# Kernel tuning notes

Hardware: AMD Instinct MI355X
Metric: run time of the kernel (lower is better)

Reference implementation:

```python
import jax, jax.numpy as jnp
import numpy as np

B, H, W, C = 2, 128, 128, 256
WS = 8            # current_window (query window)
KW = 16           # halo_window = 2*current_window
HEADS = 8
HD = C // HEADS
PRETRAIN = 8
CPB_HIDDEN = 512


def _rel_bias_consts():
    halo = (KW - WS) // 2
    coords = np.arange(1 - WS - halo, WS + halo, dtype=np.float32)  # length WS+KW-1 = 23
    tab = np.stack(np.meshgrid(coords, coords, indexing='ij'), axis=-1)  # [23,23,2]
    tab = tab * (8.0 / (PRETRAIN - 1.0))
    tab = np.sign(tab) * np.log1p(np.abs(tab)) / np.log(8.0)
    tab = tab.reshape(-1, 2).astype(np.float32)                      # [529,2]
    qi = np.arange(WS)
    qg = np.stack(np.meshgrid(qi, qi, indexing='ij')).reshape(2, -1)  # [2,64]
    ki = np.arange(KW)
    kg = np.stack(np.meshgrid(ki, ki, indexing='ij')).reshape(2, -1)  # [2,256]
    rel = qg[:, :, None] - kg[:, None] + (KW - 1)
    idx = (rel[0] * (WS + KW - 1) + rel[1]).reshape(-1).astype(np.int32)  # [64*256]
    return tab, idx

_REL_TAB, _REL_IDX = _rel_bias_consts()


def setup_inputs() -> dict:
    key = jax.random.key(0)
    ks = jax.random.split(key, 12)
    s = 0.02
    return {
        'x': jax.random.normal(ks[0], (B, H, W, C), jnp.float32),
        'w_qkv': jax.random.normal(ks[1], (C, 3 * C), jnp.float32) * s,
        'w_dw': jax.random.normal(ks[2], (3, 3, 1, 3 * C), jnp.float32) * s,  # depthwise HWIO
        'ln_g': jnp.ones((3 * C,), jnp.float32),
        'ln_b': jnp.zeros((3 * C,), jnp.float32),
        'q_bias': jnp.zeros((C,), jnp.float32),
        'v_bias': jnp.zeros((C,), jnp.float32),
        'logit_scale': jnp.full((HEADS, 1, 1), np.log(10.0), jnp.float32),
        'cpb_w1': jax.random.normal(ks[3], (2, CPB_HIDDEN), jnp.float32) * s,
        'cpb_b1': jnp.zeros((CPB_HIDDEN,), jnp.float32),
        'cpb_w2': jax.random.normal(ks[4], (CPB_HIDDEN, HEADS), jnp.float32) * s,
        'w_proj': jax.random.normal(ks[5], (C, C), jnp.float32) * s,
    }


def _l2n(t):
    # tf.math.l2_normalize with epsilon=1.55e-5
    return t * jax.lax.rsqrt(jnp.maximum(jnp.sum(t * t, -1, keepdims=True), 1.55e-5))


def reference(x, w_qkv, w_dw, ln_g, ln_b, q_bias, v_bias, logit_scale,
              cpb_w1, cpb_b1, cpb_w2, w_proj):
    nWh, nWw = H // WS, W // WS
    nW = nWh * nWw
    # qkv 1x1 conv + depthwise 3x3 + layernorm + (q,0,v) bias
    qkv = jnp.einsum('bhwc,cd->bhwd', x, w_qkv)
    qkv = jax.lax.conv_general_dilated(
        qkv, w_dw, (1, 1), 'SAME',
        dimension_numbers=('NHWC', 'HWIO', 'NHWC'), feature_group_count=3 * C)
    mu = jnp.mean(qkv, -1, keepdims=True)
    var = jnp.var(qkv, -1, keepdims=True)
    qkv = (qkv - mu) * jax.lax.rsqrt(var + 1e-5) * ln_g + ln_b
    qkv = qkv + jnp.concatenate([q_bias, jnp.zeros_like(q_bias), v_bias])
    q, kv = qkv[..., :C], qkv[..., C:]
    # window partition of q: [B*nW, heads, WS*WS, HD]
    qp = q.reshape(B, nWh, WS, nWw, WS, HEADS, HD)
    qp = qp.transpose(0, 1, 3, 5, 2, 4, 6).reshape(B * nW, HEADS, WS * WS, HD)
    # halo partition of kv: overlapping KWxKW patches, stride WS
    halo = (KW - WS) // 2
    kvp = jnp.pad(kv, ((0, 0), (halo, halo), (halo, halo), (0, 0)))
    ridx = (np.arange(nWh) * WS)[:, None] + np.arange(KW)[None]  # [nWh,KW]
    cidx = (np.arange(nWw) * WS)[:, None] + np.arange(KW)[None]  # [nWw,KW]
    kvp = kvp[:, ridx][:, :, :, cidx]               # [B,nWh,KW,nWw,KW,2C]
    kvp = kvp.transpose(0, 1, 3, 2, 4, 5).reshape(B * nW, KW * KW, 2, HEADS, HD)
    k = kvp[:, :, 0].transpose(0, 2, 1, 3)          # [B*nW, heads, KW*KW, HD]
    v = kvp[:, :, 1].transpose(0, 2, 1, 3)
    # cosine attention with clamped learned log-scale
    scale = jnp.exp(jnp.minimum(logit_scale, np.float32(np.log(100.0))))
    attn = jnp.einsum('whqd,whkd->whqk', _l2n(qp) * scale, _l2n(k))
    # continuous relative position bias (CPB MLP + gather)
    hidden = jax.nn.relu(jnp.asarray(_REL_TAB) @ cpb_w1 + cpb_b1)
    bias_tab = jax.nn.sigmoid(hidden @ cpb_w2) * 16.0        # [529, heads]
    rb = bias_tab[_REL_IDX].reshape(WS * WS, KW * KW, HEADS).transpose(2, 0, 1)
    attn = jax.nn.softmax(attn + rb[None], axis=-1)
    out = jnp.einsum('whqk,whkd->whqd', attn, v)             # [B*nW, heads, 64, HD]
    # reverse window partition
    out = out.reshape(B, nWh, nWw, HEADS, WS, WS, HD)
    out = out.transpose(0, 1, 4, 2, 5, 3, 6).reshape(B, H, W, C)
    return jnp.einsum('bhwc,cd->bhwd', out, w_proj)
```

## Files before the change

kernel.cpp:

```cpp
#include <hip/hip_runtime.h>
#include <hip/hip_bf16.h>
#include <hip/hip_fp16.h>
#include <cstddef>
#include <cstdint>

#define BB 2
#define HH 128
#define WW 128
#define CC 256
#define WSZ 8
#define KWIN 16
#define NHEADS 8
#define HD 32
#define C3 768
#define NPIX 32768
#define NWIN 512

typedef short    bf16x8 __attribute__((ext_vector_type(8)));
typedef _Float16 half8  __attribute__((ext_vector_type(8)));
typedef float    f32x4  __attribute__((ext_vector_type(4)));

#define LOG2E 1.4426950408889634f

#if __has_builtin(__builtin_amdgcn_exp2f)
#define EXP2(x) __builtin_amdgcn_exp2f(x)
#else
#define EXP2(x) __expf((x) * 0.6931471805599453f)
#endif

__device__ inline void gload_lds16(const _Float16* g, _Float16* l) {
    __builtin_amdgcn_global_load_lds(
        (const __attribute__((address_space(1))) unsigned int*)g,
        (__attribute__((address_space(3))) unsigned int*)l, 16, 0, 0);
}

__global__ __launch_bounds__(64) void cpb_kernel(const float* __restrict__ w1,
                                                 const float* __restrict__ b1,
                                                 const float* __restrict__ w2,
                                                 float* __restrict__ btab) {
    const int e = blockIdx.x;
    const int i = e / 23, j = e % 23;
    const float inv_log8 = 1.0f / logf(8.0f);
    float c0 = (float)(i - 11) * (8.0f / 7.0f);
    float c1 = (float)(j - 11) * (8.0f / 7.0f);
    float f0 = copysignf(log1pf(fabsf(c0)) * inv_log8, c0);
    float f1 = copysignf(log1pf(fabsf(c1)) * inv_log8, c1);

    const int t = threadIdx.x;
    float acc[8] = {0.f,0.f,0.f,0.f,0.f,0.f,0.f,0.f};
    for (int kk = 0; kk < 8; kk++) {
        int k = kk * 64 + t;
        float hid = f0 * w1[k] + f1 * w1[512 + k] + b1[k];
        hid = fmaxf(hid, 0.f);
        #pragma unroll
        for (int h = 0; h < 8; h++) acc[h] += hid * w2[k * 8 + h];
    }
    #pragma unroll
    for (int h = 0; h < 8; h++) {
        #pragma unroll
        for (int off = 32; off >= 1; off >>= 1) acc[h] += __shfl_xor(acc[h], off);
    }
    if (t < 8) {
        float v = acc[t];
        btab[e * 8 + t] = 16.0f / (1.0f + expf(-v));
    }
}

__global__ __launch_bounds__(256) void cvt_wdw(const float* __restrict__ src,
                                               _Float16* __restrict__ dst) {
    int i = blockIdx.x * 256 + threadIdx.x;
    if (i < 9 * C3) dst[i] = (_Float16)src[i];
}

__global__ __launch_bounds__(256) void transpose_cvt(const float* __restrict__ src,
                                                     _Float16* __restrict__ dst,
                                                     int R, int Cn) {
    __shared__ float t[32][33];
    const int bx = blockIdx.x, by = blockIdx.y;
    const int tx = threadIdx.x & 31, ty = threadIdx.x >> 5;
    #pragma unroll
    for (int i = 0; i < 4; i++) {
        int r = by * 32 + ty + i * 8;
        t[ty + i * 8][tx] = src[(size_t)r * Cn + bx * 32 + tx];
    }
    __syncthreads();
    #pragma unroll
    for (int i = 0; i < 4; i++) {
        int dr = bx * 32 + ty + i * 8;
        dst[(size_t)dr * R + by * 32 + tx] = (_Float16)t[tx][ty + i * 8];
    }
}

template <typename OT>
__global__ __launch_bounds__(256) void gemm_f16(const _Float16* __restrict__ A,
                                                const _Float16* __restrict__ Bt,
                                                OT* __restrict__ C,
                                                int M, int N, int K) {
    __shared__ _Float16 Ash[128][64];
    __shared__ _Float16 Bsh[128][64];
    const int tid = threadIdx.x;
    const int wv = tid >> 6, ln = tid & 63;
    const int quad = ln >> 4, l15 = ln & 15;
    const int rowb = blockIdx.y * 128;
    const int colb = blockIdx.x * 128;
    const int wm = (wv >> 1) * 64, wn = (wv & 1) * 64;

    const int r8 = ln >> 3, g = ln & 7;
    const int kg = g ^ r8;

    f32x4 acc[4][4] = {};
    for (int k0 = 0; k0 < K; k0 += 64) {
        #pragma unroll
        for (int i = 0; i < 4; i++) {
            const int m = wv * 32 + i * 8 + r8;
            gload_lds16(A + (size_t)(rowb + m) * K + k0 + kg * 8,
                        &Ash[wv * 32 + i * 8][0]);
            gload_lds16(Bt + (size_t)(colb + m) * K + k0 + kg * 8,
                        &Bsh[wv * 32 + i * 8][0]);
        }
        __syncthreads();
        #pragma unroll
        for (int kk = 0; kk < 2; kk++) {
            const int phys = ((kk * 4 + quad) ^ (l15 & 7)) * 8;
            half8 a[4], b[4];
            #pragma unroll
            for (int i = 0; i < 4; i++)
                a[i] = *(const half8*)&Ash[wm + i * 16 + l15][phys];
            #pragma unroll
            for (int j = 0; j < 4; j++)
                b[j] = *(const half8*)&Bsh[wn + j * 16 + l15][phys];
            #pragma unroll
            for (int i = 0; i < 4; i++)
                #pragma unroll
                for (int j = 0; j < 4; j++)
                    acc[i][j] = __builtin_amdgcn_mfma_f32_16x16x32_f16(
                        a[i], b[j], acc[i][j], 0, 0, 0);
        }
        __syncthreads();
    }
    #pragma unroll
    for (int i = 0; i < 4; i++) {
        #pragma unroll
        for (int reg = 0; reg < 4; reg++) {
            const size_t row = rowb + wm + i * 16 + quad * 4 + reg;
            #pragma unroll
            for (int j = 0; j < 4; j++) {
                C[row * N + colb + wn + j * 16 + l15] = (OT)acc[i][j][reg];
            }
        }
    }
}

__global__ __launch_bounds__(256) void gemm_qkv(const float* __restrict__ A,
                                                const _Float16* __restrict__ Bt,
                                                _Float16* __restrict__ C,
                                                int M, int N, int K) {
    __shared__ _Float16 Ash[128][64];
    __shared__ _Float16 Bsh[128][64];
    const int tid = threadIdx.x;
    const int wv = tid >> 6, ln = tid & 63;
    const int quad = ln >> 4, l15 = ln & 15;
    const int rowb = blockIdx.y * 128;
    const int colb = blockIdx.x * 128;
    const int wm = (wv >> 1) * 64, wn = (wv & 1) * 64;
    const int r8 = ln >> 3, g = ln & 7;
    const int kg = g ^ r8;

    f32x4 acc[4][4] = {};
    for (int k0 = 0; k0 < K; k0 += 64) {
        #pragma unroll
        for (int i = 0; i < 4; i++) {
            const int m = wv * 32 + i * 8 + r8;
            const float* ap = A + (size_t)(rowb + m) * K + k0 + g * 8;
            const float4 a0 = *(const float4*)ap;
            const float4 a1 = *(const float4*)(ap + 4);
            half8 hv;
            hv[0] = (_Float16)a0.x; hv[1] = (_Float16)a0.y;
            hv[2] = (_Float16)a0.z; hv[3] = (_Float16)a0.w;
            hv[4] = (_Float16)a1.x; hv[5] = (_Float16)a1.y;
            hv[6] = (_Float16)a1.z; hv[7] = (_Float16)a1.w;
            *(half8*)&Ash[wv * 32 + i * 8 + r8][kg * 8] = hv;
            gload_lds16(Bt + (size_t)(colb + m) * K + k0 + kg * 8,
                        &Bsh[wv * 32 + i * 8][0]);
        }
        __syncthreads();
        #pragma unroll
        for (int kk = 0; kk < 2; kk++) {
            const int phys = ((kk * 4 + quad) ^ (l15 & 7)) * 8;
            half8 a[4], b[4];
            #pragma unroll
            for (int i = 0; i < 4; i++)
                a[i] = *(const half8*)&Ash[wm + i * 16 + l15][phys];
            #pragma unroll
            for (int j = 0; j < 4; j++)
                b[j] = *(const half8*)&Bsh[wn + j * 16 + l15][phys];
            #pragma unroll
            for (int i = 0; i < 4; i++)
                #pragma unroll
                for (int j = 0; j < 4; j++)
                    acc[i][j] = __builtin_amdgcn_mfma_f32_16x16x32_f16(
                        a[i], b[j], acc[i][j], 0, 0, 0);
        }
        __syncthreads();
    }
    #pragma unroll
    for (int i = 0; i < 4; i++) {
        #pragma unroll
        for (int reg = 0; reg < 4; reg++) {
            const size_t row = rowb + wm + i * 16 + quad * 4 + reg;
            #pragma unroll
            for (int j = 0; j < 4; j++) {
                C[row * N + colb + wn + j * 16 + l15] = (_Float16)acc[i][j][reg];
            }
        }
    }
}

__global__ __launch_bounds__(256) void dwconv_ln(const _Float16* __restrict__ in,
                                                 const _Float16* __restrict__ wdwh,
                                                 const float* __restrict__ g,
                                                 const float* __restrict__ bt,
                                                 const float* __restrict__ qb,
                                                 const float* __restrict__ vb,
                                                 _Float16* __restrict__ out) {
    __shared__ float sred[4][8][2];

    const int t = threadIdx.x;
    const int pix0 = blockIdx.x * 8;
    const int b = pix0 >> 14, y = (pix0 >> 7) & 127, x0 = pix0 & 127;
    const int p = t & 7, gidx = t >> 3;
    const int xc = x0 + p;

    const _Float16* base[3];
    bool rok[3];
    #pragma unroll
    for (int r = 0; r < 3; r++) {
        const int yy = y + r - 1;
        rok[r] = ((unsigned)yy < 128u);
        const int yyc = yy < 0 ? 0 : (yy > 127 ? 127 : yy);
        base[r] = in + ((size_t)((b * 128 + yyc) * 128 + xc) * C3) + gidx * 8;
    }
    const bool xok0 = (xc != 0), xok2 = (xc != 127);
    const bool blk_edge = (y == 0) | (y == 127) | (x0 == 0) | (x0 == 120);

    float acc[3][8] = {};
    #pragma unroll
    for (int s = 0; s < 3; s++) {
        const int grp = gidx + s * 32;
        half8 w[9];
        #pragma unroll
        for (int tap = 0; tap < 9; tap++)
            w[tap] = *(const half8*)(wdwh + (tap * 96 + grp) * 8);
        #pragma unroll
        for (int r = 0; r < 3; r++) {
            #pragma unroll
            for (int dx = 0; dx < 3; dx++) {
                half8 v = *(const half8*)(base[r] + (dx - 1) * C3 + s * 256);
                if (blk_edge) {
                    const bool ok = rok[r] &&
                        (dx == 0 ? xok0 : (dx == 2 ? xok2 : true));
                    if (!ok) v = (half8)(_Float16)0;
                }
                const half8 wt = w[r * 3 + dx];
                #pragma unroll
                for (int i = 0; i < 8; i++)
                    acc[s][i] += (float)v[i] * (float)wt[i];
            }
        }
    }

    float ls = 0.f, lss = 0.f;
    #pragma unroll
    for (int s = 0; s < 3; s++)
        #pragma unroll
        for (int i = 0; i < 8; i++) { ls += acc[s][i]; lss += acc[s][i] * acc[s][i]; }
    ls  += __shfl_xor(ls, 8);  lss += __shfl_xor(lss, 8);
    ls  += __shfl_xor(ls, 16); lss += __shfl_xor(lss, 16);
    ls  += __shfl_xor(ls, 32); lss += __shfl_xor(lss, 32);
    const int wv = t >> 6, lnid = t & 63;
    if (lnid < 8) { sred[wv][lnid][0] = ls; sred[wv][lnid][1] = lss; }
    __syncthreads();
    const float Ssum  = sred[0][p][0] + sred[1][p][0] + sred[2][p][0] + sred[3][p][0];
    const float SSsum = sred[0][p][1] + sred[1][p][1] + sred[2][p][1] + sred[3][p][1];
    const float mu  = Ssum * (1.0f / 768.0f);
    const float var = SSsum * (1.0f / 768.0f) - mu * mu;
    const float rs  = rsqrtf(var + 1e-5f);

    const size_t obase = (size_t)(pix0 + p) * C3;
    #pragma unroll
    for (int s = 0; s < 3; s++) {
        const int ch = gidx * 8 + s * 256;
        const float4 g0 = *(const float4*)(g + ch);
        const float4 g1 = *(const float4*)(g + ch + 4);
        const float4 b0 = *(const float4*)(bt + ch);
        const float4 b1 = *(const float4*)(bt + ch + 4);
        float gg[8] = {g0.x, g0.y, g0.z, g0.w, g1.x, g1.y, g1.z, g1.w};
        float bb[8] = {b0.x, b0.y, b0.z, b0.w, b1.x, b1.y, b1.z, b1.w};
        if (s == 0) {
            const float4 e0 = *(const float4*)(qb + ch);
            const float4 e1 = *(const float4*)(qb + ch + 4);
            bb[0] += e0.x; bb[1] += e0.y; bb[2] += e0.z; bb[3] += e0.w;
            bb[4] += e1.x; bb[5] += e1.y; bb[6] += e1.z; bb[7] += e1.w;
        } else if (s == 2) {
            const float4 e0 = *(const float4*)(vb + ch - 512);
            const float4 e1 = *(const float4*)(vb + ch - 512 + 4);
            bb[0] += e0.x; bb[1] += e0.y; bb[2] += e0.z; bb[3] += e0.w;
            bb[4] += e1.x; bb[5] += e1.y; bb[6] += e1.z; bb[7] += e1.w;
        }
        half8 o;
        #pragma unroll
        for (int i = 0; i < 8; i++)
            o[i] = (_Float16)((acc[s][i] - mu) * rs * gg[i] + bb[i]);
        *(half8*)(out + obase + ch) = o;
    }
}

#define P2SHIFT 14.0f

__global__ __launch_bounds__(256) void attn_mfma(const _Float16* __restrict__ qkv,
                                                 const float* __restrict__ bias_tab,
                                                 const float* __restrict__ logit_scale,
                                                 _Float16* __restrict__ out) {
    const int blk = blockIdx.x;
    const int h = blk & 7;
    const int wid = blk >> 3;
    const int b = wid >> 8;
    const int wy = (wid >> 4) & 15;
    const int wx = wid & 15;
    const int tid = threadIdx.x;
    const int wave = tid >> 6, lane = tid & 63;
    const int quad = lane >> 4, l15 = lane & 15;

    __shared__ __align__(16) _Float16 Bf[16 * 64 * 8];
    __shared__ __align__(16) _Float16 Vt[32][264];
    __shared__ float btab[529];

    const float lscale = __expf(fminf(logit_scale[h], 4.60517019f));
    const float MshiftL2 = (lscale + 16.0f) * LOG2E - P2SHIFT;
    for (int e = tid; e < 529; e += 256)
        btab[e] = bias_tab[e * 8 + h] * LOG2E - MshiftL2;

    {
        const int j = tid;
        const int kr = j >> 4, kcc = j & 15;
        const int gy = wy * 8 - 4 + kr, gx = wx * 8 - 4 + kcc;
        const bool inb = ((unsigned)gy < 128u) && ((unsigned)gx < 128u);
        const _Float16* p = qkv +
            (((size_t)(b * 128 + (inb ? gy : 0)) * 128 + (inb ? gx : 0)) * C3) +
            256 + h * HD;
        float kreg[32];
        float s2 = 0.f;
        #pragma unroll
        for (int d8 = 0; d8 < 4; d8++) {
            half8 kk, vv;
            if (inb) { kk = *(const half8*)(p + d8 * 8); vv = *(const half8*)(p + 256 + d8 * 8); }
            else     { kk = (half8)(_Float16)0;          vv = (half8)(_Float16)0; }
            #pragma unroll
            for (int u = 0; u < 8; u++) {
                const float kf = (float)kk[u];
                kreg[d8 * 8 + u] = kf;
                s2 += kf * kf;
                Vt[d8 * 8 + u][j] = vv[u];
            }
        }
        const float r = rsqrtf(fmaxf(s2, 1.55e-5f));
        const int nt  = ((j >> 5) << 1) | ((j >> 2) & 1);
        const int pos = (((j >> 3) & 3) << 2) | (j & 3);
        #pragma unroll
        for (int d8 = 0; d8 < 4; d8++) {
            half8 hv;
            #pragma unroll
            for (int u = 0; u < 8; u++)
                hv[u] = (_Float16)(kreg[d8 * 8 + u] * r);
            *(half8*)&Bf[((nt * 64) + d8 * 16 + pos) * 8] = hv;
        }
    }

    const int qrow = wave * 16 + l15;
    const int qr = qrow >> 3, qc = qrow & 7;
    const int qy = wy * 8 + qr, qx = wx * 8 + qc;
    half8 qfrag;
    {
        const _Float16* qp = qkv + (((size_t)(b * 128 + qy) * 128 + qx) * C3) + h * HD + quad * 8;
        half8 q8 = *(const half8*)qp;
        float qf[8];
        float s2 = 0.f;
        #pragma unroll
        for (int u = 0; u < 8; u++) { qf[u] = (float)q8[u]; s2 += qf[u] * qf[u]; }
        s2 += __shfl_xor(s2, 16);
        s2 += __shfl_xor(s2, 32);
        const float rq = rsqrtf(fmaxf(s2, 1.55e-5f)) * lscale * LOG2E;
        #pragma unroll
        for (int u = 0; u < 8; u++) qfrag[u] = (_Float16)(qf[u] * rq);
    }
    __syncthreads();

    const int colbase = qc + 15 - ((quad & 1) << 3);
    const int rowq    = qr + 15 - (quad >> 1);
    float lsum = 0.f;
    f32x4 d0 = {0.f, 0.f, 0.f, 0.f};
    f32x4 d1 = {0.f, 0.f, 0.f, 0.f};
    #pragma unroll
    for (int ch = 0; ch < 8; ch++) {
        const half8 ka0 = *(const half8*)&Bf[((2 * ch)     * 64 + lane) * 8];
        const half8 ka1 = *(const half8*)&Bf[((2 * ch + 1) * 64 + lane) * 8];
        f32x4 s0 = {0.f, 0.f, 0.f, 0.f};
        f32x4 s1 = {0.f, 0.f, 0.f, 0.f};
        s0 = __builtin_amdgcn_mfma_f32_16x16x32_f16(ka0, qfrag, s0, 0, 0, 0);
        s1 = __builtin_amdgcn_mfma_f32_16x16x32_f16(ka1, qfrag, s1, 0, 0, 0);
        const float* bt = &btab[(rowq - 2 * ch) * 23 + colbase];
        half8 pa;
        #pragma unroll
        for (int r = 0; r < 4; r++) {
            const float p0 = EXP2(s0[r] + bt[-r]);
            const float p1 = EXP2(s1[r] + bt[-4 - r]);
            lsum += p0 + p1;
            pa[r]     = (_Float16)p0;
            pa[4 + r] = (_Float16)p1;
        }
        const half8 v0 = *(const half8*)&Vt[l15][ch * 32 + quad * 8];
        const half8 v1 = *(const half8*)&Vt[l15 + 16][ch * 32 + quad * 8];
        d0 = __builtin_amdgcn_mfma_f32_16x16x32_f16(pa, v0, d0, 0, 0, 0);
        d1 = __builtin_amdgcn_mfma_f32_16x16x32_f16(pa, v1, d1, 0, 0, 0);
    }

    lsum += __shfl_xor(lsum, 16);
    lsum += __shfl_xor(lsum, 32);
    const float inv = 1.0f / lsum;

    #pragma unroll
    for (int reg = 0; reg < 4; reg++) {
        const int q = quad * 4 + reg;
        const float invq = __shfl(inv, q);
        const int gq = wave * 16 + q;
        const int oqr = gq >> 3, oqc = gq & 7;
        const int oy = wy * 8 + oqr, ox = wx * 8 + oqc;
        _Float16* op = out + (((size_t)(b * 128 + oy) * 128 + ox) * CC) + h * HD;
        op[l15]      = (_Float16)(d0[reg] * invq);
        op[16 + l15] = (_Float16)(d1[reg] * invq);
    }
}

extern "C" void kernel_launch(void* const* d_in, const int* in_sizes, int n_in,
                              void* d_out, int out_size, void* d_ws, size_t ws_size,
                              hipStream_t stream) {
    const float* x           = (const float*)d_in[0];
    const float* w_qkv       = (const float*)d_in[1];
    const float* w_dw        = (const float*)d_in[2];
    const float* ln_g        = (const float*)d_in[3];
    const float* ln_b        = (const float*)d_in[4];
    const float* q_bias      = (const float*)d_in[5];
    const float* v_bias      = (const float*)d_in[6];
    const float* logit_scale = (const float*)d_in[7];
    const float* cpb_w1      = (const float*)d_in[8];
    const float* cpb_b1      = (const float*)d_in[9];
    const float* cpb_w2      = (const float*)d_in[10];
    const float* w_proj      = (const float*)d_in[11];
    float* out = (float*)d_out;

    char* ws = (char*)d_ws;
    _Float16* attnh  = (_Float16*)(ws);
    _Float16* qkvh   = (_Float16*)(ws + 16777216);
    _Float16* qkv0h  = (_Float16*)(ws + 67108864);
    _Float16* wqkvT  = (_Float16*)(ws + 117440512);
    _Float16* wprojT = (_Float16*)(ws + 117833728);
    _Float16* wdwh   = (_Float16*)(ws + 117964800);
    float*    btab   = (float*)   (ws + 117981184);

    cpb_kernel<<<529, 64, 0, stream>>>(cpb_w1, cpb_b1, cpb_w2, btab);
    cvt_wdw<<<27, 256, 0, stream>>>(w_dw, wdwh);
    transpose_cvt<<<dim3(C3 / 32, CC / 32), 256, 0, stream>>>(w_qkv, wqkvT, CC, C3);
    transpose_cvt<<<dim3(CC / 32, CC / 32), 256, 0, stream>>>(w_proj, wprojT, CC, CC);

    gemm_qkv<<<dim3(C3 / 128, NPIX / 128), 256, 0, stream>>>(
        x, wqkvT, qkv0h, NPIX, C3, CC);
    dwconv_ln<<<NPIX / 8, 256, 0, stream>>>(qkv0h, wdwh, ln_g, ln_b, q_bias,
                                            v_bias, qkvh);
    attn_mfma<<<NWIN * NHEADS, 256, 0, stream>>>(qkvh, btab, logit_scale, attnh);
    gemm_f16<float><<<dim3(CC / 128, NPIX / 128), 256, 0, stream>>>(
        attnh, wprojT, out, NPIX, CC, CC);
}
```

Measured before the change: 266.0 us.

## Stage depthwise-conv halo tile in LDS with double buffering and XOR swizzle

Measured after the change: 239.6 us. 9.9% less time.

```diff
diff --git a/kernel.cpp b/kernel.cpp
--- a/kernel.cpp
+++ b/kernel.cpp
@@ -223,44 +223,61 @@
                                                  const float* __restrict__ qb,
                                                  const float* __restrict__ vb,
                                                  _Float16* __restrict__ out) {
+    __shared__ __align__(16) _Float16 S[2][960 * 8];
     __shared__ float sred[4][8][2];
 
     const int t = threadIdx.x;
     const int pix0 = blockIdx.x * 8;
     const int b = pix0 >> 14, y = (pix0 >> 7) & 127, x0 = pix0 & 127;
     const int p = t & 7, gidx = t >> 3;
-    const int xc = x0 + p;
-
-    const _Float16* base[3];
-    bool rok[3];
-    #pragma unroll
-    for (int r = 0; r < 3; r++) {
-        const int yy = y + r - 1;
-        rok[r] = ((unsigned)yy < 128u);
-        const int yyc = yy < 0 ? 0 : (yy > 127 ? 127 : yy);
-        base[r] = in + ((size_t)((b * 128 + yyc) * 128 + xc) * C3) + gidx * 8;
-    }
-    const bool xok0 = (xc != 0), xok2 = (xc != 127);
-    const bool blk_edge = (y == 0) | (y == 127) | (x0 == 0) | (x0 == 120);
-
+
+    const _Float16* sp[4];
+    int sphys[4];
+    bool sok[4];
+    #pragma unroll
+    for (int k = 0; k < 4; k++) {
+        const int u = t + k * 256;
+        const int cell = u >> 5, grp = u & 31;
+        const int r = (cell >= 20) ? 2 : (cell >= 10 ? 1 : 0);
+        const int c = cell - r * 10;
+        const int yy = y + r - 1, xx = x0 + c - 1;
+        const bool inb = ((unsigned)yy < 128u) && ((unsigned)xx < 128u);
+        sok[k] = inb;
+        sp[k] = in + (((size_t)(b * 128 + (inb ? yy : 0)) * 128 + (inb ? xx : 0)) * C3)
+                   + grp * 8;
+        sphys[k] = (u & ~7) | ((u ^ c) & 7);
+    }
+
+    auto STAGE = [&](int s, int buf) {
+        #pragma unroll
+        for (int k = 0; k < 4; k++) {
+            if (k < 3 || t < 192) {
+                half8 v = (half8)(_Float16)0;
+                if (sok[k]) v = *(const half8*)(sp[k] + s * 256);
+                *(half8*)&S[buf][sphys[k] * 8] = v;
+            }
+        }
+    };
+
+    STAGE(0, 0);
     float acc[3][8] = {};
     #pragma unroll
     for (int s = 0; s < 3; s++) {
-        const int grp = gidx + s * 32;
+        __syncthreads();
+        if (s < 2) STAGE(s + 1, (s + 1) & 1);
+        const _Float16* Sb = &S[s & 1][0];
         half8 w[9];
         #pragma unroll
         for (int tap = 0; tap < 9; tap++)
-            w[tap] = *(const half8*)(wdwh + (tap * 96 + grp) * 8);
+            w[tap] = *(const half8*)(wdwh + (tap * 96 + s * 32 + gidx) * 8);
         #pragma unroll
         for (int r = 0; r < 3; r++) {
             #pragma unroll
             for (int dx = 0; dx < 3; dx++) {
-                half8 v = *(const half8*)(base[r] + (dx - 1) * C3 + s * 256);
-                if (blk_edge) {
-                    const bool ok = rok[r] &&
-                        (dx == 0 ? xok0 : (dx == 2 ? xok2 : true));
-                    if (!ok) v = (half8)(_Float16)0;
-                }
+                const int cc = p + dx;
+                const int u = (r * 10 + cc) * 32 + gidx;
+                const int phys = (u & ~7) | ((u ^ cc) & 7);
+                const half8 v = *(const half8*)&Sb[phys * 8];
                 const half8 wt = w[r * 3 + dx];
                 #pragma unroll
                 for (int i = 0; i < 8; i++)
```
